# Optimization experiments

Measured on AMD Instinct MI355X. Metric: run time of the kernel, lower is better.

The kernel has to match this reference:

```python
import jax, jax.numpy as jnp
import numpy as np

IN_DIM = 201
TAU = 2.0
V_TH = 1.0
SG_ALPHA = 2.0  # ATan surrogate width

# Heaviside spike with ATan surrogate gradient (spikingjelly-style)
@jax.custom_vjp
def spike(x):
    return (x >= 0.0).astype(x.dtype)

def _spike_fwd(x):
    return spike(x), x

def _spike_bwd(x, g):
    sg = (SG_ALPHA / 2.0) / (1.0 + (jnp.pi / 2.0 * SG_ALPHA * x) ** 2)
    return (g * sg,)

spike.defvjp(_spike_fwd, _spike_bwd)

def lif(v, cur):
    """LIF neuron: leaky integrate, threshold, hard reset to 0."""
    v = v + (cur - v) / TAU
    s = spike(v - V_TH)
    v = v * (1.0 - s)
    return v, s

def setup_inputs() -> dict:
    key = jax.random.key(0)
    ks = jax.random.split(key, 10)
    B, T, F = 1024, 256, 1
    def lin(k, out_d, in_d):
        return jax.random.normal(k, (out_d, in_d), jnp.float32) / np.sqrt(in_d)
    return {
        "x": jax.random.normal(ks[0], (B, T, F), jnp.float32),
        "l1_w": lin(ks[1], 64, IN_DIM), "l1_b": jnp.zeros((64,), jnp.float32),
        "r1_w1": lin(ks[2], 64, 64), "r1_b1": jnp.zeros((64,), jnp.float32),
        "r1_w2": lin(ks[3], 64, 64), "r1_b2": jnp.zeros((64,), jnp.float32),
        "r2_w1": lin(ks[4], 128, 64), "r2_b1": jnp.zeros((128,), jnp.float32),
        "r2_w2": lin(ks[5], 128, 128), "r2_b2": jnp.zeros((128,), jnp.float32),
        "r2_dw": lin(ks[6], 128, 64), "r2_db": jnp.zeros((128,), jnp.float32),
        "wv": lin(ks[7], 128, 128), "bv": jnp.zeros((128,), jnp.float32),
        "wo": lin(ks[8], 128, 128), "bo": jnp.zeros((128,), jnp.float32),
        "fc_w": lin(ks[9], 10, 128), "fc_b": jnp.zeros((10,), jnp.float32),
    }

def reference(x, l1_w, l1_b, r1_w1, r1_b1, r1_w2, r1_b2,
              r2_w1, r2_b1, r2_w2, r2_b2, r2_dw, r2_db,
              wv, bv, wo, bo, fc_w, fc_b):
    B, T, F = x.shape
    N = B * F  # effective per-step batch after reshape(-1, in_dim)
    last_start = T - IN_DIM  # window start is clamped to this

    def step(carry, t):
        v1, v2, v3, v4, v5 = carry
        start = jnp.minimum(t, last_start)
        # window x[:, start:start+IN_DIM, :].reshape(-1, IN_DIM)
        xw = jax.lax.dynamic_slice(x, (0, start, 0), (B, IN_DIM, F))
        xw = xw.reshape(N, IN_DIM)
        # layer1: Linear + spiking neuron
        h = xw @ l1_w.T + l1_b
        v1, h = lif(v1, h)
        # res_block1 (64 -> 64, identity skip)
        out = h @ r1_w1.T + r1_b1
        v2, out = lif(v2, out)
        out = out @ r1_w2.T + r1_b2
        v3, out = lif(v3, out)
        h = out + h
        # res_block2 (64 -> 128, downsample skip)
        out = h @ r2_w1.T + r2_b1
        v4, out = lif(v4, out)
        out = out @ r2_w2.T + r2_b2
        v5, out = lif(v5, out)
        h = out + (h @ r2_dw.T + r2_db)
        # MultiheadAttention with seq_len=1: softmax over one key == 1,
        # so attn(x,x,x) == out_proj(v_proj(x)) exactly.
        att = (h @ wv.T + bv) @ wo.T + bo
        y = att @ fc_w.T + fc_b  # [N, 10]
        return (v1, v2, v3, v4, v5), y

    z64 = jnp.zeros((N, 64), x.dtype)
    z128 = jnp.zeros((N, 128), x.dtype)
    init = (z64, z64, z64, z128, z128)
    _, ys = jax.lax.scan(step, init, jnp.arange(T))  # ys: [T, N, 10]
    return ys.sum(0)
```

## Files before the change

kernel.cpp:

```cpp
#include <hip/hip_runtime.h>

#define NTHREADS 1024
#define NBLOCKS 256

typedef short bf16x8 __attribute__((ext_vector_type(8)));
typedef short bf16x4 __attribute__((ext_vector_type(4)));
typedef float f32x4  __attribute__((ext_vector_type(4)));
#define MFMA16(a,b,c) __builtin_amdgcn_mfma_f32_16x16x32_bf16(a,b,c,0,0,0)

__device__ __forceinline__ void splitbf(float f, ushort& h, ushort& l) {
    unsigned u = __float_as_uint(f);
    unsigned r = u + 0x7FFFu + ((u >> 16) & 1u);
    h = (ushort)(r >> 16);
    float fl = f - __uint_as_float(((unsigned)h) << 16);
    unsigned ul = __float_as_uint(fl);
    unsigned rl = ul + 0x7FFFu + ((ul >> 16) & 1u);
    l = (ushort)(rl >> 16);
}

__device__ __forceinline__ void load_wfrag(const float* __restrict__ Wrow,
                                           bf16x8& hi, bf16x8& lo) {
    #pragma unroll
    for (int j = 0; j < 8; ++j) {
        ushort h, l;
        splitbf(Wrow[j], h, l);
        hi[j] = (short)h;
        lo[j] = (short)l;
    }
}

__device__ __forceinline__ ushort f2bf(float f) {
    return (ushort)(__float_as_uint(f) >> 16);
}

__device__ __forceinline__ void lif4(const f32x4& c, float bias,
                                     float& v, float* __restrict__ my) {
    #pragma unroll
    for (int s2 = 0; s2 < 4; ++s2) {
        float cur = c[s2] + bias;
        float vn = fmaf(0.5f, cur - v, v);
        bool fire = (vn >= 1.0f);
        v = fire ? 0.0f : vn;
        my[s2] = fire ? 1.0f : 0.0f;
    }
}

__device__ __forceinline__ void lif4u(const f32x4& c, float bias,
                                      float& v, ushort* __restrict__ my) {
    #pragma unroll
    for (int s2 = 0; s2 < 4; ++s2) {
        float cur = c[s2] + bias;
        float vn = fmaf(0.5f, cur - v, v);
        bool fire = (vn >= 1.0f);
        v = fire ? 0.0f : vn;
        my[s2] = fire ? (ushort)0x3F80 : (ushort)0;
    }
}

__device__ __forceinline__ void pack_store4(char* addr, const float* m) {
    uint2 w;
    w.x = (__float_as_uint(m[0]) >> 16) | (__float_as_uint(m[1]) & 0xFFFF0000u);
    w.y = (__float_as_uint(m[2]) >> 16) | (__float_as_uint(m[3]) & 0xFFFF0000u);
    *(uint2*)addr = w;
}

__global__ __launch_bounds__(NTHREADS, 1) void snn_oct(
    const float* __restrict__ x,
    const float* __restrict__ l1_w,  const float* __restrict__ l1_b,
    const float* __restrict__ r1_w1, const float* __restrict__ r1_b1,
    const float* __restrict__ r1_w2, const float* __restrict__ r1_b2,
    const float* __restrict__ r2_w1, const float* __restrict__ r2_b1,
    const float* __restrict__ r2_w2, const float* __restrict__ r2_b2,
    const float* __restrict__ r2_dw, const float* __restrict__ r2_db,
    const float* __restrict__ wv,    const float* __restrict__ bv,
    const float* __restrict__ wo,    const float* __restrict__ bo,
    const float* __restrict__ fc_w,  const float* __restrict__ fc_b,
    float* __restrict__ out)
{
    __shared__ __align__(16) float curpre[14 * 1024];
    __shared__ __align__(16) char sbuf[98304];

    const int tid  = threadIdx.x;
    const int blk  = blockIdx.x;
    const int lane = tid & 63;
    const int wvi  = tid >> 6;
    const int g    = lane >> 4;
    const int l16  = lane & 15;

    char* sb_s1 = sbuf;
    char* sb_cp = sbuf + 16384;
    char* sb_s2 = sbuf + 32768;
    char* sb_h  = sbuf + 49152;
    char* sb_s4 = sbuf + 65536;

    {
        float* xstage = (float*)sbuf;
        for (int idx = tid; idx < 4 * 288; idx += NTHREADS) {
            int r = idx / 288, tt2 = idx - r * 288;
            xstage[idx] = (tt2 < 256) ? x[(blk * 4 + r) * 256 + tt2] : 0.0f;
        }
        uint* whw = (uint*)(sbuf + 23296);
        uint* wlw = (uint*)(sbuf + 52992);
        for (int idx = tid; idx < 64 * 116; idx += NTHREADS) {
            int n = idx / 116, kp = idx - n * 116;
            int k0 = kp * 2;
            float f0 = (k0 < 201)     ? l1_w[n * 201 + k0]     : 0.0f;
            float f1 = (k0 + 1 < 201) ? l1_w[n * 201 + k0 + 1] : 0.0f;
            ushort h0, l0, h1, l1v;
            splitbf(f0, h0, l0); splitbf(f1, h1, l1v);
            whw[(n * 232 + k0) >> 1] = (uint)h0 | ((uint)h1 << 16);
            wlw[(n * 232 + k0) >> 1] = (uint)l0 | ((uint)l1v << 16);
        }
        if (tid < 64) ((float*)(sbuf + 82688))[tid] = l1_b[tid];
    }
    __syncthreads();

    {
        const float* xstage = (const float*)sbuf;
        for (int idx = tid; idx < 4 * 4 * 144; idx += NTHREADS) {
            int c = idx / 576;
            int rem = idx - c * 576;
            int r = rem / 144, ep = rem - r * 144;
            int i0 = ep * 2;
            int j0 = i0 + c;
            float f0 = (j0 < 288)     ? xstage[r * 288 + j0]     : 0.0f;
            float f1 = (j0 + 1 < 288) ? xstage[r * 288 + j0 + 1] : 0.0f;
            ushort h0, l0, h1, l1v;
            splitbf(f0, h0, l0); splitbf(f1, h1, l1v);
            *(uint*)(sbuf + 4608 + (c * 4 + r) * 584 + i0 * 2) =
                (uint)h0 | ((uint)h1 << 16);
            *(uint*)(sbuf + 4608 + (16 + c * 4 + r) * 584 + i0 * 2) =
                (uint)l0 | ((uint)l1v << 16);
        }
    }
    __syncthreads();

    {
        const int r1 = wvi & 3;
        const int tt = wvi >> 2;
        const int t0 = tt << 4;
        const int cc = l16 & 3;
        const char* xh_base = sbuf + 4608 + (cc * 4 + r1) * 584;
        const char* xl_base = xh_base + 16 * 584;
        const int eb = (t0 + (l16 & ~3) + g * 8) * 2;
        const char* whb = sbuf + 23296 + (l16 * 232 + g * 8) * 2;
        const char* wlb = whb + 29696;
        const float* blds = (const float*)(sbuf + 82688);

        f32x4 accp[4];
        #pragma unroll
        for (int nt = 0; nt < 4; ++nt)
            accp[nt] = *(const f32x4*)(blds + nt * 16 + g * 4);

        #pragma unroll
        for (int kt = 0; kt < 7; ++kt) {
            const int xo = eb + kt * 64;
            bf16x4 ha = *(const bf16x4*)(xh_base + xo);
            bf16x4 hb = *(const bf16x4*)(xh_base + xo + 8);
            bf16x4 la = *(const bf16x4*)(xl_base + xo);
            bf16x4 lb = *(const bf16x4*)(xl_base + xo + 8);
            bf16x8 xh8 = __builtin_shufflevector(ha, hb, 0, 1, 2, 3, 4, 5, 6, 7);
            bf16x8 xl8 = __builtin_shufflevector(la, lb, 0, 1, 2, 3, 4, 5, 6, 7);
            #pragma unroll
            for (int nt = 0; nt < 4; ++nt) {
                const int wo2 = nt * 7424 + kt * 64;
                bf16x8 wwh = *(const bf16x8*)(whb + wo2);
                bf16x8 wwl = *(const bf16x8*)(wlb + wo2);
                accp[nt] = MFMA16(wwh, xh8, accp[nt]);
                accp[nt] = MFMA16(wwh, xl8, accp[nt]);
                accp[nt] = MFMA16(wwl, xh8, accp[nt]);
            }
        }
        if (!(tt == 3 && l16 >= 8)) {
            const int t = t0 + l16;
            float* cp = curpre + (t >> 2) * 1024 + r1 * 256 + (t & 3);
            #pragma unroll
            for (int nt = 0; nt < 4; ++nt) {
                #pragma unroll
                for (int j = 0; j < 4; ++j)
                    cp[(nt * 16 + g * 4 + j) * 4] = accp[nt][j];
            }
        }
    }
    __syncthreads();

    const int XS = (l16 & 7) << 4;
    int rdA[2], rdB[4];
    #pragma unroll
    for (int kt = 0; kt < 2; ++kt)
        rdA[kt] = (l16 << 7) + (((kt << 6) | (g << 4)) ^ XS);
    #pragma unroll
    for (int kt = 0; kt < 4; ++kt)
        rdB[kt] = (l16 << 8) + (((kt << 6) | (g << 4)) ^ XS);

    int role, bt;
    if (wvi < 2)       { role = 0; bt = wvi * 2; }
    else if (wvi < 4)  { role = 1; bt = (wvi - 2) * 2; }
    else if (wvi < 6)  { role = 2; bt = (wvi - 4) * 2; }
    else if (wvi < 10) { role = 3; bt = (wvi - 6) * 2; }
    else               { role = 4; bt = wvi - 10; }

    bf16x8 wh[4], wl[4];
    float bias[2] = {0, 0};
    float bias5 = 0.0f;
    int t5 = 0;
    if (role == 1 || role == 2) {
        const float* W = (role == 1) ? r1_w1 : r1_w2;
        const float* B = (role == 1) ? r1_b1 : r1_b2;
        #pragma unroll
        for (int t = 0; t < 2; ++t) {
            #pragma unroll
            for (int kt = 0; kt < 2; ++kt)
                load_wfrag(W + ((bt + t) * 16 + l16) * 64 + kt * 32 + g * 8,
                           wh[t * 2 + kt], wl[t * 2 + kt]);
            bias[t] = B[(bt + t) * 16 + l16];
        }
    } else if (role == 3) {
        #pragma unroll
        for (int t = 0; t < 2; ++t) {
            #pragma unroll
            for (int kt = 0; kt < 2; ++kt)
                load_wfrag(r2_w1 + ((bt + t) * 16 + l16) * 64 + kt * 32 + g * 8,
                           wh[t * 2 + kt], wl[t * 2 + kt]);
            bias[t] = r2_b1[(bt + t) * 16 + l16];
        }
    } else {
        t5 = (role == 0) ? (6 + wvi) : bt;
        #pragma unroll
        for (int kt = 0; kt < 4; ++kt)
            load_wfrag(r2_w2 + (t5 * 16 + l16) * 128 + kt * 32 + g * 8,
                       wh[kt], wl[kt]);
        bias5 = r2_b2[t5 * 16 + l16];
    }

    int sto[2][4];
    {
        const int rb = (role == 3) ? 8 : 7;
        #pragma unroll
        for (int t = 0; t < 2; ++t) {
            const int cb = ((bt + t) * 16 + l16) * 2;
            #pragma unroll
            for (int s2 = 0; s2 < 4; ++s2) {
                const int row = 4 * g + s2;
                sto[t][s2] = (row << rb) + (cb ^ ((row & 7) << 4));
            }
        }
    }
    const int cpb = (g << 7) + (l16 << 3);

    float v[2] = {0, 0}, acc[2] = {0, 0};
    float v5 = 0.0f, acc5 = 0.0f;
    float cur55[2] = {0, 0};

    auto do_beat2 = [&](const int b, const int jm, const bool steady,
                        const bool sat) __attribute__((always_inline)) {
        if (role == 0) {
            #pragma unroll
            for (int u = 0; u < 2; ++u) {
                const int q = 2 * b + u;
                if (steady || q <= 63) {
                    char* dst = sb_s1 + (((2 * jm + u) & 7) << 11);
                    char* cpy = sb_cp + (((2 * jm + u) & 7) << 11) + cpb;
                    #pragma unroll
                    for (int t = 0; t < 2; ++t) {
                        const int ta = bt + t;
                        f32x4 c;
                        if (!sat && q <= 13) {
                            c = *(const f32x4*)(curpre + (q << 10) + (g << 8) +
                                                ((ta * 16 + l16) << 2));
                            if (q == 13) cur55[t] = c[3];
                        } else {
                            c[0] = cur55[t]; c[1] = cur55[t];
                            c[2] = cur55[t]; c[3] = cur55[t];
                        }
                        float my[4];
                        lif4(c, 0.0f, v[t], my);
                        #pragma unroll
                        for (int s2 = 0; s2 < 4; ++s2)
                            *(ushort*)(dst + sto[t][s2]) = f2bf(my[s2]);
                        pack_store4(cpy + ta * 512, my);
                    }
                }
            }
            #pragma unroll
            for (int u = 0; u < 2; ++u) {
                const int q = 2 * b - 8 + u;
                if (steady || q >= 0) {
                    const char* src = sb_s4 + (((2 * jm + u) & 7) << 12);
                    bf16x8 a4[4];
                    #pragma unroll
                    for (int kt = 0; kt < 4; ++kt)
                        a4[kt] = *(const bf16x8*)(src + rdB[kt]);
                    f32x4 c = {0, 0, 0, 0};
                    #pragma unroll
                    for (int kt = 0; kt < 4; ++kt) {
                        c = MFMA16(a4[kt], wh[kt], c);
                        c = MFMA16(a4[kt], wl[kt], c);
                    }
                    float my5[4];
                    lif4(c, bias5, v5, my5);
                    acc5 += (my5[0] + my5[1]) + (my5[2] + my5[3]);
                }
            }
        } else if (role == 1) {
            #pragma unroll
            for (int u = 0; u < 2; ++u) {
                const int q = 2 * b - 2 + u;
                if (steady || (q >= 0 && q <= 63)) {
                    const char* src = sb_s1 + (((2 * jm + u + 6) & 7) << 11);
                    bf16x8 a0 = *(const bf16x8*)(src + rdA[0]);
                    bf16x8 a1 = *(const bf16x8*)(src + rdA[1]);
                    char* dst = sb_s2 + (((2 * jm + u + 6) & 7) << 11);
                    #pragma unroll
                    for (int t = 0; t < 2; ++t) {
                        f32x4 c = {0, 0, 0, 0};
                        c = MFMA16(a0, wh[t*2+0], c); c = MFMA16(a0, wl[t*2+0], c);
                        c = MFMA16(a1, wh[t*2+1], c); c = MFMA16(a1, wl[t*2+1], c);
                        ushort my[4];
                        lif4u(c, bias[t], v[t], my);
                        #pragma unroll
                        for (int s2 = 0; s2 < 4; ++s2)
                            *(ushort*)(dst + sto[t][s2]) = my[s2];
                    }
                }
            }
        } else if (role == 2) {
            #pragma unroll
            for (int u = 0; u < 2; ++u) {
                const int q = 2 * b - 4 + u;
                if (steady || (q >= 0 && q <= 63)) {
                    const char* src = sb_s2 + (((2 * jm + u + 4) & 7) << 11);
                    const char* cpy = sb_cp + (((2 * jm + u + 4) & 7) << 11) + cpb;
                    bf16x8 a0 = *(const bf16x8*)(src + rdA[0]);
                    bf16x8 a1 = *(const bf16x8*)(src + rdA[1]);
                    char* dst = sb_h + (((2 * jm + u + 4) & 7) << 11);
                    #pragma unroll
                    for (int t = 0; t < 2; ++t) {
                        const int ta = bt + t;
                        f32x4 c = {0, 0, 0, 0};
                        c = MFMA16(a0, wh[t*2+0], c); c = MFMA16(a0, wl[t*2+0], c);
                        c = MFMA16(a1, wh[t*2+1], c); c = MFMA16(a1, wl[t*2+1], c);
                        float my[4];
                        lif4(c, bias[t], v[t], my);
                        const uint2 s1w = *(const uint2*)(cpy + ta * 512);
                        float hh[4];
                        hh[0] = my[0] + __uint_as_float(s1w.x << 16);
                        hh[1] = my[1] + __uint_as_float(s1w.x & 0xFFFF0000u);
                        hh[2] = my[2] + __uint_as_float(s1w.y << 16);
                        hh[3] = my[3] + __uint_as_float(s1w.y & 0xFFFF0000u);
                        acc[t] += (hh[0] + hh[1]) + (hh[2] + hh[3]);
                        #pragma unroll
                        for (int s2 = 0; s2 < 4; ++s2)
                            *(ushort*)(dst + sto[t][s2]) = f2bf(hh[s2]);
                    }
                }
            }
        } else if (role == 3) {
            #pragma unroll
            for (int u = 0; u < 2; ++u) {
                const int q = 2 * b - 6 + u;
                if (steady || (q >= 0 && q <= 63)) {
                    const char* src = sb_h + (((2 * jm + u + 2) & 7) << 11);
                    bf16x8 a0 = *(const bf16x8*)(src + rdA[0]);
                    bf16x8 a1 = *(const bf16x8*)(src + rdA[1]);
                    char* dst = sb_s4 + (((2 * jm + u + 2) & 7) << 12);
                    #pragma unroll
                    for (int t = 0; t < 2; ++t) {
                        f32x4 c = {0, 0, 0, 0};
                        c = MFMA16(a0, wh[t*2+0], c); c = MFMA16(a0, wl[t*2+0], c);
                        c = MFMA16(a1, wh[t*2+1], c); c = MFMA16(a1, wl[t*2+1], c);
                        ushort my[4];
                        lif4u(c, bias[t], v[t], my);
                        #pragma unroll
                        for (int s2 = 0; s2 < 4; ++s2)
                            *(ushort*)(dst + sto[t][s2]) = my[s2];
                    }
                }
            }
        } else {
            #pragma unroll
            for (int u = 0; u < 2; ++u) {
                const int q = 2 * b - 8 + u;
                if (steady || q >= 0) {
                    const char* src = sb_s4 + (((2 * jm + u) & 7) << 12);
                    bf16x8 a4[4];
                    #pragma unroll
                    for (int kt = 0; kt < 4; ++kt)
                        a4[kt] = *(const bf16x8*)(src + rdB[kt]);
                    f32x4 c = {0, 0, 0, 0};
                    #pragma unroll
                    for (int kt = 0; kt < 4; ++kt) {
                        c = MFMA16(a4[kt], wh[kt], c);
                        c = MFMA16(a4[kt], wl[kt], c);
                    }
                    float my[4];
                    lif4(c, bias5, v5, my);
                    acc5 += (my[0] + my[1]) + (my[2] + my[3]);
                }
            }
        }
    };

    for (int b = 0; b < 8; ++b) {
        do_beat2(b, b & 3, false, false); __syncthreads();
    }
    #pragma unroll 1
    for (int bb = 8; bb < 32; bb += 4) {
        do_beat2(bb + 0, 0, true, true); __syncthreads();
        do_beat2(bb + 1, 1, true, true); __syncthreads();
        do_beat2(bb + 2, 2, true, true); __syncthreads();
        do_beat2(bb + 3, 3, true, true); __syncthreads();
    }
    for (int b = 32; b < 36; ++b) {
        do_beat2(b, b & 3, false, true); __syncthreads();
    }

    float* scr   = curpre;
    float* S5lds = scr;
    float* Smlds = scr + 512;
    float* ubuf  = scr + 768;
    float* tmp   = scr + 896;
    float* Weff  = scr + 2176;
    float* W2eff = scr + 3456;
    float* bcon  = scr + 4096;

    if (role == 2) {
        #pragma unroll
        for (int t = 0; t < 2; ++t)
            Smlds[g * 64 + (bt + t) * 16 + l16] = acc[t];
    } else if (role == 4 || role == 0) {
        S5lds[g * 128 + t5 * 16 + l16] = acc5;
    }
    if (tid < 128) {
        float a = bo[tid];
        for (int m = 0; m < 128; ++m) a = fmaf(wo[tid * 128 + m], bv[m], a);
        ubuf[tid] = a;
    }
    for (int idx = tid; idx < 1280; idx += NTHREADS) {
        int c = idx >> 7, k = idx & 127;
        float a = 0.0f;
        for (int m = 0; m < 128; ++m) a = fmaf(fc_w[c * 128 + m], wo[m * 128 + k], a);
        tmp[idx] = a;
    }
    __syncthreads();
    for (int idx = tid; idx < 1280; idx += NTHREADS) {
        int c = idx >> 7, j = idx & 127;
        float a = 0.0f;
        for (int k = 0; k < 128; ++k) a = fmaf(tmp[c * 128 + k], wv[k * 128 + j], a);
        Weff[idx] = a;
    }
    __syncthreads();
    for (int idx = tid; idx < 640; idx += NTHREADS) {
        int c = idx >> 6, m = idx & 63;
        float a = 0.0f;
        for (int j = 0; j < 128; ++j) a = fmaf(Weff[c * 128 + j], r2_dw[j * 64 + m], a);
        W2eff[idx] = a;
    }
    if (tid < 10) {
        float a = fc_b[tid];
        for (int k = 0; k < 128; ++k) a = fmaf(fc_w[tid * 128 + k], ubuf[k], a);
        for (int j = 0; j < 128; ++j) a = fmaf(Weff[tid * 128 + j], r2_db[j], a);
        bcon[tid] = a;
    }
    __syncthreads();
    if (tid < 40) {
        int r = tid / 10, c = tid - r * 10;
        float a = 256.0f * bcon[c];
        for (int j = 0; j < 128; ++j) a = fmaf(Weff[c * 128 + j], S5lds[r * 128 + j], a);
        for (int m = 0; m < 64;  ++m) a = fmaf(W2eff[c * 64 + m], Smlds[r * 64 + m], a);
        out[(blk * 4 + r) * 10 + c] = a;
    }
}

extern "C" void kernel_launch(void* const* d_in, const int* in_sizes, int n_in,
                              void* d_out, int out_size, void* d_ws, size_t ws_size,
                              hipStream_t stream) {
    (void)in_sizes; (void)n_in; (void)d_ws; (void)ws_size; (void)out_size;
    const float* x     = (const float*)d_in[0];
    const float* l1_w  = (const float*)d_in[1];
    const float* l1_b  = (const float*)d_in[2];
    const float* r1_w1 = (const float*)d_in[3];
    const float* r1_b1 = (const float*)d_in[4];
    const float* r1_w2 = (const float*)d_in[5];
    const float* r1_b2 = (const float*)d_in[6];
    const float* r2_w1 = (const float*)d_in[7];
    const float* r2_b1 = (const float*)d_in[8];
    const float* r2_w2 = (const float*)d_in[9];
    const float* r2_b2 = (const float*)d_in[10];
    const float* r2_dw = (const float*)d_in[11];
    const float* r2_db = (const float*)d_in[12];
    const float* wv    = (const float*)d_in[13];
    const float* bv    = (const float*)d_in[14];
    const float* wo    = (const float*)d_in[15];
    const float* bo    = (const float*)d_in[16];
    const float* fc_w  = (const float*)d_in[17];
    const float* fc_b  = (const float*)d_in[18];

    snn_oct<<<dim3(NBLOCKS), dim3(NTHREADS), 0, stream>>>(
        x, l1_w, l1_b, r1_w1, r1_b1, r1_w2, r1_b2,
        r2_w1, r2_b1, r2_w2, r2_b2, r2_dw, r2_db,
        wv, bv, wo, bo, fc_w, fc_b, (float*)d_out);
}
```

Before: 76.22 us.

## Split MFMA accumulation chains, fold bias, raise priority, reassign wave roles

Splits each hi/lo MFMA accumulation into two independent chains so consecutive MFMAs no longer depend on each other, and seeds one chain with the bias instead of adding it in the LIF step. Wraps the MFMA sections in s_setprio, reorders the wave-to-role mapping across the 16 waves, and writes spikes directly as bf16 shorts. It also unrolls the epilogue weight-folding dot products with multiple accumulators to shorten their dependency chains. Summation order changes slightly, which alters floating-point rounding.

```diff
diff --git a/kernel.cpp b/kernel.cpp
--- a/kernel.cpp
+++ b/kernel.cpp
@@ -33,35 +33,26 @@
     return (ushort)(__float_as_uint(f) >> 16);
 }
 
-__device__ __forceinline__ void lif4(const f32x4& c, float bias,
+__device__ __forceinline__ void lif4(const f32x4& c,
                                      float& v, float* __restrict__ my) {
     #pragma unroll
     for (int s2 = 0; s2 < 4; ++s2) {
-        float cur = c[s2] + bias;
-        float vn = fmaf(0.5f, cur - v, v);
+        float vn = fmaf(0.5f, c[s2] - v, v);
         bool fire = (vn >= 1.0f);
         v = fire ? 0.0f : vn;
         my[s2] = fire ? 1.0f : 0.0f;
     }
 }
 
-__device__ __forceinline__ void lif4u(const f32x4& c, float bias,
+__device__ __forceinline__ void lif4u(const f32x4& c,
                                       float& v, ushort* __restrict__ my) {
     #pragma unroll
     for (int s2 = 0; s2 < 4; ++s2) {
-        float cur = c[s2] + bias;
-        float vn = fmaf(0.5f, cur - v, v);
+        float vn = fmaf(0.5f, c[s2] - v, v);
         bool fire = (vn >= 1.0f);
         v = fire ? 0.0f : vn;
         my[s2] = fire ? (ushort)0x3F80 : (ushort)0;
     }
-}
-
-__device__ __forceinline__ void pack_store4(char* addr, const float* m) {
-    uint2 w;
-    w.x = (__float_as_uint(m[0]) >> 16) | (__float_as_uint(m[1]) & 0xFFFF0000u);
-    w.y = (__float_as_uint(m[2]) >> 16) | (__float_as_uint(m[3]) & 0xFFFF0000u);
-    *(uint2*)addr = w;
 }
 
 __global__ __launch_bounds__(NTHREADS, 1) void snn_oct(
@@ -139,8 +130,8 @@
         const int r1 = wvi & 3;
         const int tt = wvi >> 2;
         const int t0 = tt << 4;
-        const int cc = l16 & 3;
-        const char* xh_base = sbuf + 4608 + (cc * 4 + r1) * 584;
+        const int cc2 = l16 & 3;
+        const char* xh_base = sbuf + 4608 + (cc2 * 4 + r1) * 584;
         const char* xl_base = xh_base + 16 * 584;
         const int eb = (t0 + (l16 & ~3) + g * 8) * 2;
         const char* whb = sbuf + 23296 + (l16 * 232 + g * 8) * 2;
@@ -194,11 +185,24 @@
         rdB[kt] = (l16 << 8) + (((kt << 6) | (g << 4)) ^ XS);
 
     int role, bt;
-    if (wvi < 2)       { role = 0; bt = wvi * 2; }
-    else if (wvi < 4)  { role = 1; bt = (wvi - 2) * 2; }
-    else if (wvi < 6)  { role = 2; bt = (wvi - 4) * 2; }
-    else if (wvi < 10) { role = 3; bt = (wvi - 6) * 2; }
-    else               { role = 4; bt = wvi - 10; }
+    switch (wvi) {
+        case 0:  role = 0; bt = 0; break;
+        case 1:  role = 0; bt = 2; break;
+        case 2:  role = 1; bt = 0; break;
+        case 3:  role = 1; bt = 2; break;
+        case 4:  role = 3; bt = 0; break;
+        case 5:  role = 3; bt = 2; break;
+        case 6:  role = 2; bt = 0; break;
+        case 7:  role = 2; bt = 2; break;
+        case 8:  role = 4; bt = 0; break;
+        case 9:  role = 4; bt = 1; break;
+        case 10: role = 3; bt = 4; break;
+        case 11: role = 3; bt = 6; break;
+        case 12: role = 4; bt = 2; break;
+        case 13: role = 4; bt = 3; break;
+        case 14: role = 4; bt = 4; break;
+        default: role = 4; bt = 5; break;
+    }
 
     bf16x8 wh[4], wl[4];
     float bias[2] = {0, 0};
@@ -273,12 +277,15 @@
                             c[0] = cur55[t]; c[1] = cur55[t];
                             c[2] = cur55[t]; c[3] = cur55[t];
                         }
-                        float my[4];
-                        lif4(c, 0.0f, v[t], my);
+                        ushort my[4];
+                        lif4u(c, v[t], my);
                         #pragma unroll
                         for (int s2 = 0; s2 < 4; ++s2)
-                            *(ushort*)(dst + sto[t][s2]) = f2bf(my[s2]);
-                        pack_store4(cpy + ta * 512, my);
+                            *(ushort*)(dst + sto[t][s2]) = my[s2];
+                        uint2 w;
+                        w.x = (uint)my[0] | ((uint)my[1] << 16);
+                        w.y = (uint)my[2] | ((uint)my[3] << 16);
+                        *(uint2*)(cpy + ta * 512) = w;
                     }
                 }
             }
@@ -291,14 +298,18 @@
                     #pragma unroll
                     for (int kt = 0; kt < 4; ++kt)
                         a4[kt] = *(const bf16x8*)(src + rdB[kt]);
-                    f32x4 c = {0, 0, 0, 0};
+                    f32x4 c0 = {bias5, bias5, bias5, bias5};
+                    f32x4 c1 = {0, 0, 0, 0};
+                    __builtin_amdgcn_s_setprio(1);
                     #pragma unroll
                     for (int kt = 0; kt < 4; ++kt) {
-                        c = MFMA16(a4[kt], wh[kt], c);
-                        c = MFMA16(a4[kt], wl[kt], c);
-                    }
+                        c0 = MFMA16(a4[kt], wh[kt], c0);
+                        c1 = MFMA16(a4[kt], wl[kt], c1);
+                    }
+                    __builtin_amdgcn_s_setprio(0);
+                    f32x4 c = c0 + c1;
                     float my5[4];
-                    lif4(c, bias5, v5, my5);
+                    lif4(c, v5, my5);
                     acc5 += (my5[0] + my5[1]) + (my5[2] + my5[3]);
                 }
             }
@@ -311,13 +322,21 @@
                     bf16x8 a0 = *(const bf16x8*)(src + rdA[0]);
                     bf16x8 a1 = *(const bf16x8*)(src + rdA[1]);
                     char* dst = sb_s2 + (((2 * jm + u + 6) & 7) << 11);
-                    #pragma unroll
-                    for (int t = 0; t < 2; ++t) {
-                        f32x4 c = {0, 0, 0, 0};
-                        c = MFMA16(a0, wh[t*2+0], c); c = MFMA16(a0, wl[t*2+0], c);
-                        c = MFMA16(a1, wh[t*2+1], c); c = MFMA16(a1, wl[t*2+1], c);
+                    f32x4 cc[2];
+                    __builtin_amdgcn_s_setprio(1);
+                    #pragma unroll
+                    for (int t = 0; t < 2; ++t) {
+                        f32x4 c0 = {bias[t], bias[t], bias[t], bias[t]};
+                        f32x4 c1 = {0, 0, 0, 0};
+                        c0 = MFMA16(a0, wh[t*2+0], c0); c1 = MFMA16(a0, wl[t*2+0], c1);
+                        c0 = MFMA16(a1, wh[t*2+1], c0); c1 = MFMA16(a1, wl[t*2+1], c1);
+                        cc[t] = c0 + c1;
+                    }
+                    __builtin_amdgcn_s_setprio(0);
+                    #pragma unroll
+                    for (int t = 0; t < 2; ++t) {
                         ushort my[4];
-                        lif4u(c, bias[t], v[t], my);
+                        lif4u(cc[t], v[t], my);
                         #pragma unroll
                         for (int s2 = 0; s2 < 4; ++s2)
                             *(ushort*)(dst + sto[t][s2]) = my[s2];
@@ -334,14 +353,22 @@
                     bf16x8 a0 = *(const bf16x8*)(src + rdA[0]);
                     bf16x8 a1 = *(const bf16x8*)(src + rdA[1]);
                     char* dst = sb_h + (((2 * jm + u + 4) & 7) << 11);
+                    f32x4 cc[2];
+                    __builtin_amdgcn_s_setprio(1);
+                    #pragma unroll
+                    for (int t = 0; t < 2; ++t) {
+                        f32x4 c0 = {bias[t], bias[t], bias[t], bias[t]};
+                        f32x4 c1 = {0, 0, 0, 0};
+                        c0 = MFMA16(a0, wh[t*2+0], c0); c1 = MFMA16(a0, wl[t*2+0], c1);
+                        c0 = MFMA16(a1, wh[t*2+1], c0); c1 = MFMA16(a1, wl[t*2+1], c1);
+                        cc[t] = c0 + c1;
+                    }
+                    __builtin_amdgcn_s_setprio(0);
                     #pragma unroll
                     for (int t = 0; t < 2; ++t) {
                         const int ta = bt + t;
-                        f32x4 c = {0, 0, 0, 0};
-                        c = MFMA16(a0, wh[t*2+0], c); c = MFMA16(a0, wl[t*2+0], c);
-                        c = MFMA16(a1, wh[t*2+1], c); c = MFMA16(a1, wl[t*2+1], c);
                         float my[4];
-                        lif4(c, bias[t], v[t], my);
+                        lif4(cc[t], v[t], my);
                         const uint2 s1w = *(const uint2*)(cpy + ta * 512);
                         float hh[4];
                         hh[0] = my[0] + __uint_as_float(s1w.x << 16);
@@ -364,13 +391,21 @@
                     bf16x8 a0 = *(const bf16x8*)(src + rdA[0]);
                     bf16x8 a1 = *(const bf16x8*)(src + rdA[1]);
                     char* dst = sb_s4 + (((2 * jm + u + 2) & 7) << 12);
-                    #pragma unroll
-                    for (int t = 0; t < 2; ++t) {
-                        f32x4 c = {0, 0, 0, 0};
-                        c = MFMA16(a0, wh[t*2+0], c); c = MFMA16(a0, wl[t*2+0], c);
-                        c = MFMA16(a1, wh[t*2+1], c); c = MFMA16(a1, wl[t*2+1], c);
+                    f32x4 cc[2];
+                    __builtin_amdgcn_s_setprio(1);
+                    #pragma unroll
+                    for (int t = 0; t < 2; ++t) {
+                        f32x4 c0 = {bias[t], bias[t], bias[t], bias[t]};
+                        f32x4 c1 = {0, 0, 0, 0};
+                        c0 = MFMA16(a0, wh[t*2+0], c0); c1 = MFMA16(a0, wl[t*2+0], c1);
+                        c0 = MFMA16(a1, wh[t*2+1], c0); c1 = MFMA16(a1, wl[t*2+1], c1);
+                        cc[t] = c0 + c1;
+                    }
+                    __builtin_amdgcn_s_setprio(0);
+                    #pragma unroll
+                    for (int t = 0; t < 2; ++t) {
                         ushort my[4];
-                        lif4u(c, bias[t], v[t], my);
+                        lif4u(cc[t], v[t], my);
                         #pragma unroll
                         for (int s2 = 0; s2 < 4; ++s2)
                             *(ushort*)(dst + sto[t][s2]) = my[s2];
@@ -387,14 +422,18 @@
                     #pragma unroll
                     for (int kt = 0; kt < 4; ++kt)
                         a4[kt] = *(const bf16x8*)(src + rdB[kt]);
-                    f32x4 c = {0, 0, 0, 0};
+                    f32x4 c0 = {bias5, bias5, bias5, bias5};
+                    f32x4 c1 = {0, 0, 0, 0};
+                    __builtin_amdgcn_s_setprio(1);
                     #pragma unroll
                     for (int kt = 0; kt < 4; ++kt) {
-                        c = MFMA16(a4[kt], wh[kt], c);
-                        c = MFMA16(a4[kt], wl[kt], c);
-                    }
+                        c0 = MFMA16(a4[kt], wh[kt], c0);
+                        c1 = MFMA16(a4[kt], wl[kt], c1);
+                    }
+                    __builtin_amdgcn_s_setprio(0);
+                    f32x4 c = c0 + c1;
                     float my[4];
-                    lif4(c, bias5, v5, my);
+                    lif4(c, v5, my);
                     acc5 += (my[0] + my[1]) + (my[2] + my[3]);
                 }
             }
@@ -432,43 +471,80 @@
         S5lds[g * 128 + t5 * 16 + l16] = acc5;
     }
     if (tid < 128) {
-        float a = bo[tid];
-        for (int m = 0; m < 128; ++m) a = fmaf(wo[tid * 128 + m], bv[m], a);
-        ubuf[tid] = a;
+        float a0 = 0, a1 = 0, a2 = 0, a3 = 0;
+        for (int m = 0; m < 128; m += 4) {
+            a0 = fmaf(wo[tid * 128 + m],     bv[m],     a0);
+            a1 = fmaf(wo[tid * 128 + m + 1], bv[m + 1], a1);
+            a2 = fmaf(wo[tid * 128 + m + 2], bv[m + 2], a2);
+            a3 = fmaf(wo[tid * 128 + m + 3], bv[m + 3], a3);
+        }
+        ubuf[tid] = bo[tid] + ((a0 + a1) + (a2 + a3));
     }
     for (int idx = tid; idx < 1280; idx += NTHREADS) {
         int c = idx >> 7, k = idx & 127;
-        float a = 0.0f;
-        for (int m = 0; m < 128; ++m) a = fmaf(fc_w[c * 128 + m], wo[m * 128 + k], a);
-        tmp[idx] = a;
+        float a0 = 0, a1 = 0, a2 = 0, a3 = 0;
+        for (int m = 0; m < 128; m += 4) {
+            a0 = fmaf(fc_w[c * 128 + m],     wo[(m)     * 128 + k], a0);
+            a1 = fmaf(fc_w[c * 128 + m + 1], wo[(m + 1) * 128 + k], a1);
+            a2 = fmaf(fc_w[c * 128 + m + 2], wo[(m + 2) * 128 + k], a2);
+            a3 = fmaf(fc_w[c * 128 + m + 3], wo[(m + 3) * 128 + k], a3);
+        }
+        tmp[idx] = (a0 + a1) + (a2 + a3);
     }
     __syncthreads();
     for (int idx = tid; idx < 1280; idx += NTHREADS) {
         int c = idx >> 7, j = idx & 127;
-        float a = 0.0f;
-        for (int k = 0; k < 128; ++k) a = fmaf(tmp[c * 128 + k], wv[k * 128 + j], a);
-        Weff[idx] = a;
+        float a0 = 0, a1 = 0, a2 = 0, a3 = 0;
+        for (int k = 0; k < 128; k += 4) {
+            a0 = fmaf(tmp[c * 128 + k],     wv[(k)     * 128 + j], a0);
+            a1 = fmaf(tmp[c * 128 + k + 1], wv[(k + 1) * 128 + j], a1);
+            a2 = fmaf(tmp[c * 128 + k + 2], wv[(k + 2) * 128 + j], a2);
+            a3 = fmaf(tmp[c * 128 + k + 3], wv[(k + 3) * 128 + j], a3);
+        }
+        Weff[idx] = (a0 + a1) + (a2 + a3);
     }
     __syncthreads();
     for (int idx = tid; idx < 640; idx += NTHREADS) {
         int c = idx >> 6, m = idx & 63;
-        float a = 0.0f;
-        for (int j = 0; j < 128; ++j) a = fmaf(Weff[c * 128 + j], r2_dw[j * 64 + m], a);
-        W2eff[idx] = a;
+        float a0 = 0, a1 = 0, a2 = 0, a3 = 0;
+        for (int j = 0; j < 128; j += 4) {
+            a0 = fmaf(Weff[c * 128 + j],     r2_dw[(j)     * 64 + m], a0);
+            a1 = fmaf(Weff[c * 128 + j + 1], r2_dw[(j + 1) * 64 + m], a1);
+            a2 = fmaf(Weff[c * 128 + j + 2], r2_dw[(j + 2) * 64 + m], a2);
+            a3 = fmaf(Weff[c * 128 + j + 3], r2_dw[(j + 3) * 64 + m], a3);
+        }
+        W2eff[idx] = (a0 + a1) + (a2 + a3);
     }
     if (tid < 10) {
-        float a = fc_b[tid];
-        for (int k = 0; k < 128; ++k) a = fmaf(fc_w[tid * 128 + k], ubuf[k], a);
-        for (int j = 0; j < 128; ++j) a = fmaf(Weff[tid * 128 + j], r2_db[j], a);
-        bcon[tid] = a;
+        float a0 = 0, a1 = 0;
+        for (int k = 0; k < 128; k += 2) {
+            a0 = fmaf(fc_w[tid * 128 + k],     ubuf[k],     a0);
+            a1 = fmaf(fc_w[tid * 128 + k + 1], ubuf[k + 1], a1);
+        }
+        float b0 = 0, b1 = 0;
+        for (int j = 0; j < 128; j += 2) {
+            b0 = fmaf(Weff[tid * 128 + j],     r2_db[j],     b0);
+            b1 = fmaf(Weff[tid * 128 + j + 1], r2_db[j + 1], b1);
+        }
+        bcon[tid] = fc_b[tid] + (a0 + a1) + (b0 + b1);
     }
     __syncthreads();
     if (tid < 40) {
         int r = tid / 10, c = tid - r * 10;
-        float a = 256.0f * bcon[c];
-        for (int j = 0; j < 128; ++j) a = fmaf(Weff[c * 128 + j], S5lds[r * 128 + j], a);
-        for (int m = 0; m < 64;  ++m) a = fmaf(W2eff[c * 64 + m], Smlds[r * 64 + m], a);
-        out[(blk * 4 + r) * 10 + c] = a;
+        float a0 = 0, a1 = 0, a2 = 0, a3 = 0;
+        for (int j = 0; j < 128; j += 4) {
+            a0 = fmaf(Weff[c * 128 + j],     S5lds[r * 128 + j],     a0);
+            a1 = fmaf(Weff[c * 128 + j + 1], S5lds[r * 128 + j + 1], a1);
+            a2 = fmaf(Weff[c * 128 + j + 2], S5lds[r * 128 + j + 2], a2);
+            a3 = fmaf(Weff[c * 128 + j + 3], S5lds[r * 128 + j + 3], a3);
+        }
+        float b0 = 0, b1 = 0;
+        for (int m = 0; m < 64; m += 2) {
+            b0 = fmaf(W2eff[c * 64 + m],     Smlds[r * 64 + m],     b0);
+            b1 = fmaf(W2eff[c * 64 + m + 1], Smlds[r * 64 + m + 1], b1);
+        }
+        out[(blk * 4 + r) * 10 + c] =
+            256.0f * bcon[c] + ((a0 + a1) + (a2 + a3)) + (b0 + b1);
     }
 }
 
```

Result: slower. 106.1 us (+39.2%).
